# Kernel tuning notes

Hardware: AMD Instinct MI355X
Metric: run time of the kernel (lower is better)

The kernel has to match this reference:

```python
import jax, jax.numpy as jnp
import numpy as np

SEQ, B, XD = 2048, 4, 16
D, NH, DFF, L, M = 256, 8, 512, 2, 1024
DH = D // NH
NEG_INF = -1e9  # finite stand-in for -inf (same softmax result, grad-safe)


def setup_inputs() -> dict:
    key = jax.random.key(0)
    ks = iter(jax.random.split(key, 40))

    def w(shape, s=0.02):
        return jax.random.normal(next(ks), shape, dtype=jnp.float32) * s

    return {
        "x": jax.random.normal(next(ks), (SEQ, B, XD), dtype=jnp.float32),
        "y": jax.random.normal(next(ks), (SEQ, B), dtype=jnp.float32),
        "single_eval_pos": M,
        "xenc_w": w((D, XD)), "xenc_b": w((D,)),
        "yenc_w": w((D, 1)), "yenc_b": w((D,)),
        "in_proj_w": w((L, 3 * D, D)), "in_proj_b": w((L, 3 * D)),
        "out_proj_w": w((L, D, D)), "out_proj_b": w((L, D)),
        "ln1_g": jnp.ones((L, D), jnp.float32), "ln1_b": jnp.zeros((L, D), jnp.float32),
        "lin1_w": w((L, DFF, D)), "lin1_b": w((L, DFF)),
        "lin2_w": w((L, D, DFF)), "lin2_b": w((L, D)),
        "ln2_g": jnp.ones((L, D), jnp.float32), "ln2_b": jnp.zeros((L, D), jnp.float32),
        "head_w1": w((DFF, D)), "head_b1": w((DFF,)),
        "head_w2": w((1, DFF)), "head_b2": w((1,)),
    }


def _layer_norm(x, g, b, eps=1e-5):
    mu = jnp.mean(x, axis=-1, keepdims=True)
    var = jnp.var(x, axis=-1, keepdims=True)
    return (x - mu) * jax.lax.rsqrt(var + eps) * g + b


def _forward(x, y, M_, p):
    seq, batch = y.shape
    x_src = x @ p["xenc_w"].T + p["xenc_b"]                     # [seq, b, D]
    y_src = y[..., None] @ p["yenc_w"].T + p["yenc_b"]           # [seq, b, D]
    tokens = jnp.concatenate([x_src[:M_] + y_src[:M_], x_src[M_:]], axis=0)

    # prefix-block + diagonal mask: keep (j < M) or (i == j)
    i = jnp.arange(seq)
    keep = (i[None, :] < M_) | (i[:, None] == i[None, :])
    mask = jnp.where(keep, 0.0, NEG_INF).astype(tokens.dtype)    # [seq, seq]

    h = tokens
    for l in range(p["in_proj_w"].shape[0]):
        qkv = h @ p["in_proj_w"][l].T + p["in_proj_b"][l]        # [seq, b, 3D]
        q, k, v = jnp.split(qkv, 3, axis=-1)
        to_heads = lambda t: t.reshape(seq, batch, NH, DH).transpose(1, 2, 0, 3)
        q, k, v = to_heads(q), to_heads(k), to_heads(v)          # [b, h, s, dh]
        scores = jnp.einsum("bhqd,bhkd->bhqk", q, k) / np.float32(np.sqrt(DH)) + mask
        attn = jax.nn.softmax(scores, axis=-1)
        o = jnp.einsum("bhqk,bhkd->bhqd", attn, v)
        o = o.transpose(2, 0, 1, 3).reshape(seq, batch, D)
        o = o @ p["out_proj_w"][l].T + p["out_proj_b"][l]
        h = _layer_norm(h + o, p["ln1_g"][l], p["ln1_b"][l])      # post-norm
        ff = jax.nn.gelu(h @ p["lin1_w"][l].T + p["lin1_b"][l], approximate=False)
        ff = ff @ p["lin2_w"][l].T + p["lin2_b"][l]
        h = _layer_norm(h + ff, p["ln2_g"][l], p["ln2_b"][l])

    q_out = h[M_:]                                               # [seq-M, b, D]
    hid = jax.nn.gelu(q_out @ p["head_w1"].T + p["head_b1"], approximate=False)
    return hid @ p["head_w2"].T + p["head_b2"]                   # [seq-M, b, 1]


def reference(x, y, single_eval_pos, xenc_w, xenc_b, yenc_w, yenc_b,
              in_proj_w, in_proj_b, out_proj_w, out_proj_b,
              ln1_g, ln1_b, lin1_w, lin1_b, lin2_w, lin2_b, ln2_g, ln2_b,
              head_w1, head_b1, head_w2, head_b2):
    p = dict(xenc_w=xenc_w, xenc_b=xenc_b, yenc_w=yenc_w, yenc_b=yenc_b,
             in_proj_w=in_proj_w, in_proj_b=in_proj_b,
             out_proj_w=out_proj_w, out_proj_b=out_proj_b,
             ln1_g=ln1_g, ln1_b=ln1_b, lin1_w=lin1_w, lin1_b=lin1_b,
             lin2_w=lin2_w, lin2_b=lin2_b, ln2_g=ln2_g, ln2_b=ln2_b,
             head_w1=head_w1, head_b1=head_b1, head_w2=head_w2, head_b2=head_b2)
    return _forward(x, y, int(single_eval_pos), p)
```

## Files before the change

kernel.cpp:

```cpp
#include <hip/hip_runtime.h>
#include <hip/hip_bf16.h>
#include <math.h>

#define SEQ    2048
#define BATCH  4
#define XDIM   16
#define DMODEL 256
#define NHEAD  8
#define DH     32
#define DFF    512
#define NLAYER 2
#define MPOS   1024
#define ROWS   (SEQ*BATCH)

#define ATT_SCALE 0.17677669529663687f

typedef __attribute__((ext_vector_type(8))) short bf16x8;
typedef __attribute__((ext_vector_type(4))) float f32x4;

__device__ __forceinline__ float gelu_exact(float x) {
    return 0.5f * x * (1.0f + erff(x * 0.70710678118654752f));
}
__device__ __forceinline__ short f2bf(float f) {
    unsigned int u = __float_as_uint(f);
    u += 0x7FFFu + ((u >> 16) & 1u);
    return (short)(u >> 16);
}
__device__ __forceinline__ float bf2f(unsigned short u) {
    return __uint_as_float(((unsigned int)u) << 16);
}
__device__ __forceinline__ void gload16(const unsigned short* g, unsigned short* l) {
    __builtin_amdgcn_global_load_lds(
        (const __attribute__((address_space(1))) unsigned int*)g,
        (__attribute__((address_space(3))) unsigned int*)l, 16, 0, 0);
}
#define VMWAIT(N) asm volatile("s_waitcnt vmcnt(" #N ")" ::: "memory")
__device__ __forceinline__ void pipe_barrier() {
    __builtin_amdgcn_sched_barrier(0);
    __builtin_amdgcn_s_barrier();
    __builtin_amdgcn_sched_barrier(0);
}

__global__ __launch_bounds__(256) void encode_cast(
    const float* __restrict__ x, const float* __restrict__ y,
    const float* __restrict__ xw, const float* __restrict__ xb,
    const float* __restrict__ yw, const float* __restrict__ yb,
    float* __restrict__ h, unsigned short* __restrict__ hb,
    const float* __restrict__ s0, const float* __restrict__ s1,
    const float* __restrict__ s2, const float* __restrict__ s3,
    const float* __restrict__ s4,
    unsigned short* __restrict__ d0, unsigned short* __restrict__ d1,
    unsigned short* __restrict__ d2, unsigned short* __restrict__ d3,
    unsigned short* __restrict__ d4)
{
    if (blockIdx.x < ROWS/4) {
        int g = blockIdx.x;
        int d = threadIdx.x;
        __shared__ float xs[4][XDIM];
        __shared__ float ys[4];
        if (d < 64) xs[d>>4][d&15] = x[(size_t)(g*4 + (d>>4))*XDIM + (d&15)];
        if (d < 4)  ys[d] = y[g*4 + d];
        __syncthreads();
        float wreg[XDIM];
        #pragma unroll
        for (int k = 0; k < XDIM; ++k) wreg[k] = xw[d*XDIM + k];
        const float xbv = xb[d], ywv = yw[d], ybv = yb[d];
        const bool train = (g < MPOS);
        #pragma unroll
        for (int r = 0; r < 4; ++r) {
            int row = g*4 + r;
            float acc = xbv;
            #pragma unroll
            for (int k = 0; k < XDIM; ++k) acc = fmaf(xs[r][k], wreg[k], acc);
            if (train) acc += ys[r]*ywv + ybv;
            h[(size_t)row*DMODEL + d]  = acc;
            hb[(size_t)row*DMODEL + d] = (unsigned short)f2bf(acc);
        }
        return;
    }
    int i = (blockIdx.x - ROWS/4)*256 + threadIdx.x;
    if (i >= 147456) return;
    const float* s; unsigned short* d; int off;
    if      (i <  49152) { s = s0; d = d0; off = i; }
    else if (i <  65536) { s = s1; d = d1; off = i - 49152; }
    else if (i <  98304) { s = s2; d = d2; off = i - 65536; }
    else if (i < 131072) { s = s3; d = d3; off = i - 98304; }
    else                 { s = s4; d = d4; off = i - 131072; }
    float4 a = *(const float4*)(s + (size_t)off*8);
    float4 c = *(const float4*)(s + (size_t)off*8 + 4);
    ushort4 u0, u1;
    u0.x=(unsigned short)f2bf(a.x); u0.y=(unsigned short)f2bf(a.y);
    u0.z=(unsigned short)f2bf(a.z); u0.w=(unsigned short)f2bf(a.w);
    u1.x=(unsigned short)f2bf(c.x); u1.y=(unsigned short)f2bf(c.y);
    u1.z=(unsigned short)f2bf(c.z); u1.w=(unsigned short)f2bf(c.w);
    *(ushort4*)(d + (size_t)off*8)     = u0;
    *(ushort4*)(d + (size_t)off*8 + 4) = u1;
}

__global__ __launch_bounds__(512) void gemm_qkv(
    const unsigned short* __restrict__ A, const unsigned short* __restrict__ B,
    const float* __restrict__ bias,
    unsigned short* __restrict__ Qg, unsigned short* __restrict__ Kg,
    unsigned short* __restrict__ Vg, int K)
{
    __shared__ unsigned short As[2][128][64];
    __shared__ unsigned short Bs[2][64][64];
    int tid  = threadIdx.x;
    int w    = tid >> 6, lane = tid & 63;
    int col  = lane & 15, quad = lane >> 4;
    int wr   = w >> 1, wc = w & 1;
    int u    = blockIdx.x >> 3, xcd = blockIdx.x & 7;
    int by   = xcd*8 + u/12, bx = u%12;
    int m0   = by * 128, n0 = bx * 64;
    int l8   = lane >> 3;
    int c8s  = (((lane & 7) ^ l8) * 8);

    f32x4 acc[2][2];
    #pragma unroll
    for (int i = 0; i < 2; ++i)
        #pragma unroll
        for (int j = 0; j < 2; ++j) acc[i][j] = (f32x4){0.f,0.f,0.f,0.f};

    const unsigned short* ga = A + (size_t)(m0 + w*16 + l8)*K + c8s;
    const unsigned short* gb = B + (size_t)(n0 + w*8  + l8)*K + c8s;
    const int NS = K / 64;

    gload16(ga,                 &As[0][w*16    ][0]);
    gload16(ga + (size_t)8*K,   &As[0][w*16 + 8][0]);
    gload16(gb,                 &Bs[0][w*8     ][0]);

    for (int s = 0; s < NS; ++s) {
        VMWAIT(0);
        pipe_barrier();
        if (s + 1 < NS) {
            int k2 = (s + 1) * 64;
            int nb = (s + 1) & 1;
            gload16(ga + k2,               &As[nb][w*16    ][0]);
            gload16(ga + k2 + (size_t)8*K, &As[nb][w*16 + 8][0]);
            gload16(gb + k2,               &Bs[nb][w*8     ][0]);
        }
        int cur = s & 1;
        #pragma unroll
        for (int kk = 0; kk < 2; ++kk) {
            const int so = (((kk*4 + quad) ^ (col & 7)) * 8);
            bf16x8 af[2], bfr[2];
            #pragma unroll
            for (int i = 0; i < 2; ++i) af[i]  = *(const bf16x8*)&As[cur][wr*32 + i*16 + col][so];
            #pragma unroll
            for (int j = 0; j < 2; ++j) bfr[j] = *(const bf16x8*)&Bs[cur][wc*32 + j*16 + col][so];
            #pragma unroll
            for (int i = 0; i < 2; ++i)
                #pragma unroll
                for (int j = 0; j < 2; ++j)
                    acc[i][j] = __builtin_amdgcn_mfma_f32_16x16x32_bf16(bfr[j], af[i], acc[i][j], 0, 0, 0);
        }
    }

    int region = n0 >> 8;
    if (region < 2) {
        #pragma unroll
        for (int i = 0; i < 2; ++i) {
            int m = m0 + wr*32 + i*16 + col;
            int s = m >> 2, bidx = m & 3;
            #pragma unroll
            for (int j = 0; j < 2; ++j) {
                int ng = n0 + wc*32 + j*16 + quad*4;
                float4 bi = *(const float4*)&bias[ng];
                ushort4 uu;
                uu.x=(unsigned short)f2bf(acc[i][j][0] + bi.x);
                uu.y=(unsigned short)f2bf(acc[i][j][1] + bi.y);
                uu.z=(unsigned short)f2bf(acc[i][j][2] + bi.z);
                uu.w=(unsigned short)f2bf(acc[i][j][3] + bi.w);
                int np = ng - (region << 8);
                int hh = np >> 5, d = np & 31;
                int bh = bidx*NHEAD + hh;
                if (region == 0)
                    *(ushort4*)(Qg + ((size_t)(bh*SEQ + s))*DH + d) = uu;
                else
                    *(ushort4*)(Kg + ((size_t)(bh*SEQ + s))*DH + d) = uu;
            }
        }
    } else {
        __syncthreads();
        unsigned short* T3 = (unsigned short*)As;
        #pragma unroll
        for (int i = 0; i < 2; ++i) {
            int mi = wr*32 + i*16 + col;
            int ss = mi >> 2, bidx = mi & 3;
            #pragma unroll
            for (int j = 0; j < 2; ++j) {
                int ni = wc*32 + j*16 + quad*4;
                float4 bi = *(const float4*)&bias[n0 + ni];
                T3[((ni    )*4 + bidx)*32 + ss] = (unsigned short)f2bf(acc[i][j][0] + bi.x);
                T3[((ni + 1)*4 + bidx)*32 + ss] = (unsigned short)f2bf(acc[i][j][1] + bi.y);
                T3[((ni + 2)*4 + bidx)*32 + ss] = (unsigned short)f2bf(acc[i][j][2] + bi.z);
                T3[((ni + 3)*4 + bidx)*32 + ss] = (unsigned short)f2bf(acc[i][j][3] + bi.w);
            }
        }
        __syncthreads();
        int sBase = m0 >> 2;
        #pragma unroll
        for (int r = 0; r < 2; ++r) {
            int chunk = tid + 512*r;
            int l = chunk >> 2, p = chunk & 3;
            int d = l & 31, hh_l = (l >> 5) & 1, bidx = l >> 6;
            int ni = hh_l*32 + d;
            int hh = ((n0 & 255) + ni) >> 5;
            int bh = bidx*NHEAD + hh;
            uint4 val = *(const uint4*)&T3[(ni*4 + bidx)*32 + p*8];
            *(uint4*)(Vg + ((size_t)(bh*DH + d))*SEQ + sBase + p*8) = val;
        }
    }
}

__global__ __launch_bounds__(512) void attn_mfma(
    const unsigned short* __restrict__ Qg,
    const unsigned short* __restrict__ Kg,
    const unsigned short* __restrict__ Vg,
    unsigned short* __restrict__ o)
{
    const int id  = blockIdx.x;
    const int sl  = id >> 3;
    const int bh  = (id & 7) * 4 + (sl >> 4);
    const int qt2 = sl & 15;
    const int h   = bh & 7;
    const int b   = bh >> 3;
    const int q0A = qt2 * 64;
    const int q0B = MPOS + qt2 * 64;
    const int tid  = threadIdx.x;
    const int w    = tid >> 6;
    const int ws   = w & 3;
    const int grp  = w >> 2;
    const int lane = tid & 63;
    const int col  = lane & 15;
    const int quad = lane >> 4;

    __shared__ unsigned short Kt[2][128][40];
    __shared__ unsigned short Vt[2][32][136];
    __shared__ unsigned short Pt[8][16][136];

    const int q0 = grp ? q0B : q0A;
    const int q  = q0 + 16*ws + col;
    bf16x8 qf = *(const bf16x8*)(Qg + ((size_t)(bh*SEQ + q))*DH + quad*8);

    f32x4 O0 = {0.f,0.f,0.f,0.f};
    f32x4 O1 = {0.f,0.f,0.f,0.f};
    float lsum = 0.f;

    const int kRow = tid >> 2,  kCh = (tid & 3) * 8;
    const int vD   = tid >> 4,  vCh = (tid & 15) * 8;

    uint4 kreg = *(const uint4*)(Kg + ((size_t)(bh*SEQ + kRow))*DH + kCh);
    uint4 vreg = *(const uint4*)(Vg + ((size_t)(bh*DH + vD))*SEQ + vCh);

    for (int kt = 0; kt < 8; ++kt) {
        const int p = kt & 1;
        *(uint4*)&Kt[p][kRow][kCh] = kreg;
        *(uint4*)&Vt[p][vD][vCh]   = vreg;
        __syncthreads();
        if (kt < 7) {
            int kn = (kt + 1) * 128;
            kreg = *(const uint4*)(Kg + ((size_t)(bh*SEQ + kn + kRow))*DH + kCh);
            vreg = *(const uint4*)(Vg + ((size_t)(bh*DH + vD))*SEQ + kn + vCh);
        } else {
            if (kRow < 64)
                kreg = *(const uint4*)(Kg + ((size_t)(bh*SEQ + q0B + kRow))*DH + kCh);
            if (vCh < 64)
                vreg = *(const uint4*)(Vg + ((size_t)(bh*DH + vD))*SEQ + q0B + vCh);
        }

        #pragma unroll
        for (int mt = 0; mt < 8; ++mt) {
            bf16x8 kf = *(const bf16x8*)&Kt[p][mt*16 + col][quad*8];
            f32x4 st = {0.f,0.f,0.f,0.f};
            st = __builtin_amdgcn_mfma_f32_16x16x32_bf16(kf, qf, st, 0, 0, 0);
            ushort4 pw;
            #pragma unroll
            for (int i = 0; i < 4; ++i) {
                float pv = __expf(st[i]*ATT_SCALE);
                unsigned short us = (unsigned short)f2bf(pv);
                ((unsigned short*)&pw)[i] = us;
                lsum += bf2f(us);
            }
            *(ushort4*)&Pt[w][col][mt*16 + quad*4] = pw;
        }
        #pragma unroll
        for (int c = 0; c < 4; ++c) {
            bf16x8 v0 = *(const bf16x8*)&Vt[p][col     ][c*32 + quad*8];
            bf16x8 v1 = *(const bf16x8*)&Vt[p][col + 16][c*32 + quad*8];
            bf16x8 pf = *(const bf16x8*)&Pt[w][col][c*32 + quad*8];
            O0 = __builtin_amdgcn_mfma_f32_16x16x32_bf16(v0, pf, O0, 0, 0, 0);
            O1 = __builtin_amdgcn_mfma_f32_16x16x32_bf16(v1, pf, O1, 0, 0, 0);
        }
    }

    if (kRow < 64) *(uint4*)&Kt[0][kRow][kCh] = kreg;
    if (vCh < 64)  *(uint4*)&Vt[0][vD][vCh]   = vreg;
    __syncthreads();
    if (grp == 1) {
        #pragma unroll
        for (int mt = 0; mt < 4; ++mt) {
            bf16x8 kf = *(const bf16x8*)&Kt[0][mt*16 + col][quad*8];
            f32x4 st = {0.f,0.f,0.f,0.f};
            st = __builtin_amdgcn_mfma_f32_16x16x32_bf16(kf, qf, st, 0, 0, 0);
            ushort4 pw;
            #pragma unroll
            for (int i = 0; i < 4; ++i) {
                float pv = __expf(st[i]*ATT_SCALE);
                if (mt*16 + quad*4 + i != 16*ws + col) pv = 0.f;
                unsigned short us = (unsigned short)f2bf(pv);
                ((unsigned short*)&pw)[i] = us;
                lsum += bf2f(us);
            }
            *(ushort4*)&Pt[w][col][mt*16 + quad*4] = pw;
        }
        #pragma unroll
        for (int c = 0; c < 2; ++c) {
            bf16x8 v0 = *(const bf16x8*)&Vt[0][col     ][c*32 + quad*8];
            bf16x8 v1 = *(const bf16x8*)&Vt[0][col + 16][c*32 + quad*8];
            bf16x8 pf = *(const bf16x8*)&Pt[w][col][c*32 + quad*8];
            O0 = __builtin_amdgcn_mfma_f32_16x16x32_bf16(v0, pf, O0, 0, 0, 0);
            O1 = __builtin_amdgcn_mfma_f32_16x16x32_bf16(v1, pf, O1, 0, 0, 0);
        }
    }

    lsum += __shfl_xor(lsum, 16, 64);
    lsum += __shfl_xor(lsum, 32, 64);
    float inv = 1.0f / lsum;
    ushort4 u0, u1;
    #pragma unroll
    for (int i = 0; i < 4; ++i) {
        ((unsigned short*)&u0)[i] = (unsigned short)f2bf(O0[i]*inv);
        ((unsigned short*)&u1)[i] = (unsigned short)f2bf(O1[i]*inv);
    }
    unsigned short* op = o + ((size_t)(q*BATCH + b))*DMODEL + h*DH;
    *(ushort4*)(op + quad*4)      = u0;
    *(ushort4*)(op + 16 + quad*4) = u1;
}

__global__ __launch_bounds__(512) void mlp_fused(
    const unsigned short* __restrict__ attb,
    const unsigned short* __restrict__ Wout, const float* __restrict__ ob,
    const float* __restrict__ g1, const float* __restrict__ be1,
    const unsigned short* __restrict__ W1, const float* __restrict__ fb1,
    const unsigned short* __restrict__ W2, const float* __restrict__ fb2,
    const float* __restrict__ g2, const float* __restrict__ be2,
    float* __restrict__ h, unsigned short* __restrict__ hb,
    const unsigned short* __restrict__ Wh1, const float* __restrict__ hb1,
    const float* __restrict__ hw2, const float* __restrict__ hb2,
    float* __restrict__ out, int doHead)
{
    __shared__ unsigned short Bs[3][256][64];
    __shared__ __align__(16) unsigned char smem_u[33280];
    __shared__ unsigned short Ht[2][16][264];
    __shared__ float sP[2][8][16], qP[2][8][16];

    typedef unsigned short AsT[2][16][64];
    AsT* As = reinterpret_cast<AsT*>(smem_u);
    typedef unsigned short PtT[16][520];
    PtT* Pt = reinterpret_cast<PtT*>(smem_u);

    const int tid  = threadIdx.x;
    const int w    = tid >> 6;
    const int lane = tid & 63;
    const int col  = lane & 15;
    const int quad = lane >> 4;
    const int l8   = lane >> 3;
    const int c8s  = (((lane & 7) ^ l8) * 8);
    const int bid  = blockIdx.x;
    const int m0a  = bid * 16;
    const int m0b  = 4096 + bid * 16;
    const int ma   = m0a + col;
    const int mb   = m0b + col;

    float resid[2][2][4];

    {
        f32x4 acc[2][2];
        #pragma unroll
        for (int g = 0; g < 2; ++g)
            #pragma unroll
            for (int j = 0; j < 2; ++j) acc[g][j] = (f32x4){0.f,0.f,0.f,0.f};

        const int gr = w >> 1;
        const unsigned short* gaw = attb + (size_t)((gr ? m0b : m0a) + (w&1)*8 + l8)*DMODEL + c8s;
        const unsigned short* gb  = Wout + (size_t)(w*32 + l8)*DMODEL + c8s;
        const int NS = DMODEL / 64;

        #pragma unroll
        for (int pb = 0; pb < 2; ++pb) {
            int k = pb * 64;
            if (w < 4) gload16(gaw + k, &As[pb][gr][(w&1)*8][0]);
            #pragma unroll
            for (int t = 0; t < 4; ++t)
                gload16(gb + k + (size_t)(t*8)*DMODEL, &Bs[pb][w*32 + t*8][0]);
        }
        int bcur = 0;
        for (int s = 0; s < NS; ++s) {
            if (s == NS - 1)      { VMWAIT(0); }
            else if (w < 4)       { VMWAIT(5); }
            else                  { VMWAIT(4); }
            pipe_barrier();
            if (s + 2 < NS) {
                int bpre = bcur + 2; if (bpre >= 3) bpre -= 3;
                int k2 = (s + 2) * 64;
                if (w < 4) gload16(gaw + k2, &As[bpre][gr][(w&1)*8][0]);
                #pragma unroll
                for (int t = 0; t < 4; ++t)
                    gload16(gb + k2 + (size_t)(t*8)*DMODEL, &Bs[bpre][w*32 + t*8][0]);
            }
            #pragma unroll
            for (int kk = 0; kk < 2; ++kk) {
                const int so = (((kk*4 + quad) ^ (col & 7)) * 8);
                bf16x8 af0 = *(const bf16x8*)&As[bcur][0][col][so];
                bf16x8 af1 = *(const bf16x8*)&As[bcur][1][col][so];
                #pragma unroll
                for (int j = 0; j < 2; ++j) {
                    bf16x8 bfr = *(const bf16x8*)&Bs[bcur][w*32 + j*16 + col][so];
                    acc[0][j] = __builtin_amdgcn_mfma_f32_16x16x32_bf16(bfr, af0, acc[0][j], 0, 0, 0);
                    acc[1][j] = __builtin_amdgcn_mfma_f32_16x16x32_bf16(bfr, af1, acc[1][j], 0, 0, 0);
                }
            }
            bcur = (bcur == 2) ? 0 : bcur + 1;
        }

        float ssum[2] = {0.f, 0.f}, qsum[2] = {0.f, 0.f};
        #pragma unroll
        for (int g = 0; g < 2; ++g) {
            int m = g ? mb : ma;
            #pragma unroll
            for (int j = 0; j < 2; ++j) {
                int n = w*32 + j*16 + quad*4;
                float4 bi = *(const float4*)&ob[n];
                float4 hv = *(const float4*)&h[(size_t)m*DMODEL + n];
                #pragma unroll
                for (int i = 0; i < 4; ++i) {
                    float val = acc[g][j][i] + ((const float*)&bi)[i] + ((const float*)&hv)[i];
                    resid[g][j][i] = val;
                    ssum[g] += val; qsum[g] += val*val;
                }
            }
        }
        #pragma unroll
        for (int g = 0; g < 2; ++g) {
            ssum[g] += __shfl_xor(ssum[g], 16, 64); ssum[g] += __shfl_xor(ssum[g], 32, 64);
            qsum[g] += __shfl_xor(qsum[g], 16, 64); qsum[g] += __shfl_xor(qsum[g], 32, 64);
        }
        if (quad == 0) {
            sP[0][w][col] = ssum[0]; qP[0][w][col] = qsum[0];
            sP[1][w][col] = ssum[1]; qP[1][w][col] = qsum[1];
        }
        __syncthreads();
        #pragma unroll
        for (int g = 0; g < 2; ++g) {
            float st = 0.f, qt = 0.f;
            #pragma unroll
            for (int ww = 0; ww < 8; ++ww) { st += sP[g][ww][col]; qt += qP[g][ww][col]; }
            float mu   = st * (1.0f/DMODEL);
            float var  = qt * (1.0f/DMODEL) - mu*mu;
            float rstd = rsqrtf(var + 1e-5f);
            #pragma unroll
            for (int j = 0; j < 2; ++j) {
                int n = w*32 + j*16 + quad*4;
                float4 gv = *(const float4*)&g1[n];
                float4 bv = *(const float4*)&be1[n];
                ushort4 u;
                #pragma unroll
                for (int i = 0; i < 4; ++i) {
                    float o = (resid[g][j][i]-mu)*rstd*((const float*)&gv)[i] + ((const float*)&bv)[i];
                    resid[g][j][i] = o;
                    ((unsigned short*)&u)[i] = (unsigned short)f2bf(o);
                }
                *(ushort4*)&Ht[g][col][n] = u;
            }
        }
        __syncthreads();
    }

    #pragma unroll 1
    for (int nh = 0; nh < 2; ++nh) {
        f32x4 acc[2][2];
        #pragma unroll
        for (int g = 0; g < 2; ++g)
            #pragma unroll
            for (int j = 0; j < 2; ++j) acc[g][j] = (f32x4){0.f,0.f,0.f,0.f};
        const unsigned short* gb = W1 + (size_t)(nh*256 + w*32 + l8)*DMODEL + c8s;
        const int NS = DMODEL / 64;

        #pragma unroll
        for (int pb = 0; pb < 2; ++pb)
            #pragma unroll
            for (int t = 0; t < 4; ++t)
                gload16(gb + pb*64 + (size_t)(t*8)*DMODEL, &Bs[pb][w*32 + t*8][0]);

        int bcur = 0;
        for (int s = 0; s < NS; ++s) {
            if (s == NS - 1) { VMWAIT(0); } else { VMWAIT(4); }
            if (s + 2 < NS) {
                int bpre = bcur + 2; if (bpre >= 3) bpre -= 3;
                int k2 = (s + 2) * 64;
                #pragma unroll
                for (int t = 0; t < 4; ++t)
                    gload16(gb + k2 + (size_t)(t*8)*DMODEL, &Bs[bpre][w*32 + t*8][0]);
            }
            #pragma unroll
            for (int kk = 0; kk < 2; ++kk) {
                const int so = (((kk*4 + quad) ^ (col & 7)) * 8);
                bf16x8 af0 = *(const bf16x8*)&Ht[0][col][s*64 + kk*32 + quad*8];
                bf16x8 af1 = *(const bf16x8*)&Ht[1][col][s*64 + kk*32 + quad*8];
                #pragma unroll
                for (int j = 0; j < 2; ++j) {
                    bf16x8 bfr = *(const bf16x8*)&Bs[bcur][w*32 + j*16 + col][so];
                    acc[0][j] = __builtin_amdgcn_mfma_f32_16x16x32_bf16(bfr, af0, acc[0][j], 0, 0, 0);
                    acc[1][j] = __builtin_amdgcn_mfma_f32_16x16x32_bf16(bfr, af1, acc[1][j], 0, 0, 0);
                }
            }
            bcur = (bcur == 2) ? 0 : bcur + 1;
        }
        #pragma unroll
        for (int g = 0; g < 2; ++g)
            #pragma unroll
            for (int j = 0; j < 2; ++j) {
                int n2 = nh*256 + w*32 + j*16 + quad*4;
                float4 bi = *(const float4*)&fb1[n2];
                ushort4 u;
                #pragma unroll
                for (int i = 0; i < 4; ++i)
                    ((unsigned short*)&u)[i] = (unsigned short)f2bf(gelu_exact(acc[g][j][i] + ((const float*)&bi)[i]));
                *(ushort4*)&Pt[g][col][n2] = u;
            }
    }

    {
        __syncthreads();
        f32x4 acc[2][2];
        #pragma unroll
        for (int g = 0; g < 2; ++g)
            #pragma unroll
            for (int j = 0; j < 2; ++j) acc[g][j] = (f32x4){0.f,0.f,0.f,0.f};
        const unsigned short* gb = W2 + (size_t)(w*32 + l8)*DFF + c8s;
        const int NS = DFF / 64;

        #pragma unroll
        for (int pb = 0; pb < 2; ++pb)
            #pragma unroll
            for (int t = 0; t < 4; ++t)
                gload16(gb + pb*64 + (size_t)(t*8)*DFF, &Bs[pb][w*32 + t*8][0]);

        int bcur = 0;
        for (int s = 0; s < NS; ++s) {
            if (s == NS - 1) { VMWAIT(0); } else { VMWAIT(4); }
            if (s + 2 < NS) {
                int bpre = bcur + 2; if (bpre >= 3) bpre -= 3;
                int k2 = (s + 2) * 64;
                #pragma unroll
                for (int t = 0; t < 4; ++t)
                    gload16(gb + k2 + (size_t)(t*8)*DFF, &Bs[bpre][w*32 + t*8][0]);
            }
            #pragma unroll
            for (int kk = 0; kk < 2; ++kk) {
                const int so = (((kk*4 + quad) ^ (col & 7)) * 8);
                bf16x8 af0 = *(const bf16x8*)&Pt[0][col][s*64 + kk*32 + quad*8];
                bf16x8 af1 = *(const bf16x8*)&Pt[1][col][s*64 + kk*32 + quad*8];
                #pragma unroll
                for (int j = 0; j < 2; ++j) {
                    bf16x8 bfr = *(const bf16x8*)&Bs[bcur][w*32 + j*16 + col][so];
                    acc[0][j] = __builtin_amdgcn_mfma_f32_16x16x32_bf16(bfr, af0, acc[0][j], 0, 0, 0);
                    acc[1][j] = __builtin_amdgcn_mfma_f32_16x16x32_bf16(bfr, af1, acc[1][j], 0, 0, 0);
                }
            }
            bcur = (bcur == 2) ? 0 : bcur + 1;
        }

        float ssum[2] = {0.f, 0.f}, qsum[2] = {0.f, 0.f};
        #pragma unroll
        for (int g = 0; g < 2; ++g)
            #pragma unroll
            for (int j = 0; j < 2; ++j) {
                int n = w*32 + j*16 + quad*4;
                float4 bi = *(const float4*)&fb2[n];
                #pragma unroll
                for (int i = 0; i < 4; ++i) {
                    float val = acc[g][j][i] + ((const float*)&bi)[i] + resid[g][j][i];
                    resid[g][j][i] = val;
                    ssum[g] += val; qsum[g] += val*val;
                }
            }
        #pragma unroll
        for (int g = 0; g < 2; ++g) {
            ssum[g] += __shfl_xor(ssum[g], 16, 64); ssum[g] += __shfl_xor(ssum[g], 32, 64);
            qsum[g] += __shfl_xor(qsum[g], 16, 64); qsum[g] += __shfl_xor(qsum[g], 32, 64);
        }
        if (quad == 0) {
            sP[0][w][col] = ssum[0]; qP[0][w][col] = qsum[0];
            sP[1][w][col] = ssum[1]; qP[1][w][col] = qsum[1];
        }
        __syncthreads();
        #pragma unroll
        for (int g = 0; g < 2; ++g) {
            int m = g ? mb : ma;
            float st = 0.f, qt = 0.f;
            #pragma unroll
            for (int ww = 0; ww < 8; ++ww) { st += sP[g][ww][col]; qt += qP[g][ww][col]; }
            float mu   = st * (1.0f/DMODEL);
            float var  = qt * (1.0f/DMODEL) - mu*mu;
            float rstd = rsqrtf(var + 1e-5f);
            #pragma unroll
            for (int j = 0; j < 2; ++j) {
                int n = w*32 + j*16 + quad*4;
                float4 gv = *(const float4*)&g2[n];
                float4 bv = *(const float4*)&be2[n];
                float4 o;
                ushort4 u;
                #pragma unroll
                for (int i = 0; i < 4; ++i) {
                    float ov = (resid[g][j][i]-mu)*rstd*((const float*)&gv)[i] + ((const float*)&bv)[i];
                    ((float*)&o)[i] = ov;
                    ((unsigned short*)&u)[i] = (unsigned short)f2bf(ov);
                }
                *(float4*)&h[(size_t)m*DMODEL + n] = o;
                *(ushort4*)(hb + (size_t)m*DMODEL + n) = u;
                *(ushort4*)&Ht[g][col][n] = u;
            }
        }
        __syncthreads();
    }

    if (doHead) {
        float sdot = 0.f;
        #pragma unroll 1
        for (int nh = 0; nh < 2; ++nh) {
            f32x4 acc[2];
            #pragma unroll
            for (int j = 0; j < 2; ++j) acc[j] = (f32x4){0.f,0.f,0.f,0.f};
            const unsigned short* gb = Wh1 + (size_t)(nh*256 + w*32 + l8)*DMODEL + c8s;
            const int NS = DMODEL / 64;

            #pragma unroll
            for (int pb = 0; pb < 2; ++pb)
                #pragma unroll
                for (int t = 0; t < 4; ++t)
                    gload16(gb + pb*64 + (size_t)(t*8)*DMODEL, &Bs[pb][w*32 + t*8][0]);

            int bcur = 0;
            for (int s = 0; s < NS; ++s) {
                if (s == NS - 1) { VMWAIT(0); } else { VMWAIT(4); }
                if (s + 2 < NS) {
                    int bpre = bcur + 2; if (bpre >= 3) bpre -= 3;
                    int k2 = (s + 2) * 64;
                    #pragma unroll
                    for (int t = 0; t < 4; ++t)
                        gload16(gb + k2 + (size_t)(t*8)*DMODEL, &Bs[bpre][w*32 + t*8][0]);
                }
                #pragma unroll
                for (int kk = 0; kk < 2; ++kk) {
                    const int so = (((kk*4 + quad) ^ (col & 7)) * 8);
                    bf16x8 af = *(const bf16x8*)&Ht[1][col][s*64 + kk*32 + quad*8];
                    #pragma unroll
                    for (int j = 0; j < 2; ++j) {
                        bf16x8 bfr = *(const bf16x8*)&Bs[bcur][w*32 + j*16 + col][so];
                        acc[j] = __builtin_amdgcn_mfma_f32_16x16x32_bf16(bfr, af, acc[j], 0, 0, 0);
                    }
                }
                bcur = (bcur == 2) ? 0 : bcur + 1;
            }
            #pragma unroll
            for (int j = 0; j < 2; ++j) {
                int n2 = nh*256 + w*32 + j*16 + quad*4;
                float4 b1v = *(const float4*)&hb1[n2];
                float4 w2v = *(const float4*)&hw2[n2];
                #pragma unroll
                for (int i = 0; i < 4; ++i)
                    sdot += gelu_exact(acc[j][i] + ((const float*)&b1v)[i]) * ((const float*)&w2v)[i];
            }
        }
        sdot += __shfl_xor(sdot, 16, 64); sdot += __shfl_xor(sdot, 32, 64);
        if (quad == 0) sP[0][w][col] = sdot;
        __syncthreads();
        if (tid < 16) {
            float r = hb2[0];
            #pragma unroll
            for (int ww = 0; ww < 8; ++ww) r += sP[0][ww][tid];
            out[bid*16 + tid] = r;
        }
    }
}

extern "C" void kernel_launch(void* const* d_in, const int* in_sizes, int n_in,
                              void* d_out, int out_size, void* d_ws, size_t ws_size,
                              hipStream_t stream)
{
    const float* x        = (const float*)d_in[0];
    const float* y        = (const float*)d_in[1];
    const float* xenc_w   = (const float*)d_in[3];
    const float* xenc_b   = (const float*)d_in[4];
    const float* yenc_w   = (const float*)d_in[5];
    const float* yenc_b   = (const float*)d_in[6];
    const float* in_proj_w  = (const float*)d_in[7];
    const float* in_proj_b  = (const float*)d_in[8];
    const float* out_proj_w = (const float*)d_in[9];
    const float* out_proj_b = (const float*)d_in[10];
    const float* ln1_g    = (const float*)d_in[11];
    const float* ln1_b    = (const float*)d_in[12];
    const float* lin1_w   = (const float*)d_in[13];
    const float* lin1_b   = (const float*)d_in[14];
    const float* lin2_w   = (const float*)d_in[15];
    const float* lin2_b   = (const float*)d_in[16];
    const float* ln2_g    = (const float*)d_in[17];
    const float* ln2_b    = (const float*)d_in[18];
    const float* head_w1  = (const float*)d_in[19];
    const float* head_b1  = (const float*)d_in[20];
    const float* head_w2  = (const float*)d_in[21];
    const float* head_b2  = (const float*)d_in[22];
    float* out = (float*)d_out;

    float* ws  = (float*)d_ws;
    float* h    = ws;
    unsigned short* hb    = (unsigned short*)(h + (size_t)ROWS*DMODEL);
    unsigned short* attb  = hb    + (size_t)ROWS*DMODEL;
    unsigned short* Qg    = attb  + (size_t)ROWS*DMODEL;
    unsigned short* Kg    = Qg    + (size_t)BATCH*NHEAD*SEQ*DH;
    unsigned short* Vg    = Kg    + (size_t)BATCH*NHEAD*SEQ*DH;
    unsigned short* Wqkv  = Vg    + (size_t)BATCH*NHEAD*SEQ*DH;
    unsigned short* Wout  = Wqkv  + (size_t)NLAYER*3*DMODEL*DMODEL;
    unsigned short* Wl1   = Wout  + (size_t)NLAYER*DMODEL*DMODEL;
    unsigned short* Wl2   = Wl1   + (size_t)NLAYER*DFF*DMODEL;
    unsigned short* Wh1   = Wl2   + (size_t)NLAYER*DMODEL*DFF;

    encode_cast<<<ROWS/4 + 576, 256, 0, stream>>>(
        x, y, xenc_w, xenc_b, yenc_w, yenc_b, h, hb,
        in_proj_w, out_proj_w, lin1_w, lin2_w, head_w1,
        Wqkv, Wout, Wl1, Wl2, Wh1);

    for (int l = 0; l < NLAYER; ++l) {
        gemm_qkv<<<768, 512, 0, stream>>>(
            hb, Wqkv + (size_t)l*3*DMODEL*DMODEL, in_proj_b + l*3*DMODEL,
            Qg, Kg, Vg, DMODEL);
        attn_mfma<<<512, 512, 0, stream>>>(Qg, Kg, Vg, attb);
        mlp_fused<<<256, 512, 0, stream>>>(
            attb,
            Wout + (size_t)l*DMODEL*DMODEL, out_proj_b + l*DMODEL,
            ln1_g + l*DMODEL, ln1_b + l*DMODEL,
            Wl1 + (size_t)l*DFF*DMODEL, lin1_b + l*DFF,
            Wl2 + (size_t)l*DMODEL*DFF, lin2_b + l*DMODEL,
            ln2_g + l*DMODEL, ln2_b + l*DMODEL,
            h, hb,
            Wh1, head_b1, head_w2, head_b2,
            out, (l == NLAYER-1) ? 1 : 0);
    }
}
```

Baseline: 222.9 us.

## Preload full B tile in QKV GEMM and give each wave private A rows

The QKV projection GEMM now loads the whole 64x256 B (weight) slice into shared memory once up front. Each wave then streams its own 16 rows of A into a private shared buffer, which removes the per-iteration block-wide barrier and the B double-buffering. Each wave computes a 16x64 output strip with four MFMAs per k-chunk instead of a 2x2 layout. The cost is larger shared-memory use per block and waves that no longer share A fragments, and the V-transpose epilogue now relies on T3 aliasing the resized As buffer.

```diff
diff --git a/kernel.cpp b/kernel.cpp
--- a/kernel.cpp
+++ b/kernel.cpp
@@ -103,99 +103,94 @@
     unsigned short* __restrict__ Qg, unsigned short* __restrict__ Kg,
     unsigned short* __restrict__ Vg, int K)
 {
-    __shared__ unsigned short As[2][128][64];
-    __shared__ unsigned short Bs[2][64][64];
+    __shared__ unsigned short Bsf[4][64][64];
+    __shared__ unsigned short As[8][16][64];
     int tid  = threadIdx.x;
     int w    = tid >> 6, lane = tid & 63;
     int col  = lane & 15, quad = lane >> 4;
-    int wr   = w >> 1, wc = w & 1;
     int u    = blockIdx.x >> 3, xcd = blockIdx.x & 7;
     int by   = xcd*8 + u/12, bx = u%12;
     int m0   = by * 128, n0 = bx * 64;
     int l8   = lane >> 3;
     int c8s  = (((lane & 7) ^ l8) * 8);
 
-    f32x4 acc[2][2];
+    f32x4 acc[4];
     #pragma unroll
-    for (int i = 0; i < 2; ++i)
-        #pragma unroll
-        for (int j = 0; j < 2; ++j) acc[i][j] = (f32x4){0.f,0.f,0.f,0.f};
+    for (int j = 0; j < 4; ++j) acc[j] = (f32x4){0.f,0.f,0.f,0.f};
 
     const unsigned short* ga = A + (size_t)(m0 + w*16 + l8)*K + c8s;
-    const unsigned short* gb = B + (size_t)(n0 + w*8  + l8)*K + c8s;
     const int NS = K / 64;
 
-    gload16(ga,                 &As[0][w*16    ][0]);
-    gload16(ga + (size_t)8*K,   &As[0][w*16 + 8][0]);
-    gload16(gb,                 &Bs[0][w*8     ][0]);
+    {
+        int seg = w >> 1;
+        int r0  = (w & 1) * 32;
+        const unsigned short* gbw = B + (size_t)(n0 + r0 + l8)*K + seg*64 + c8s;
+        #pragma unroll
+        for (int t = 0; t < 4; ++t)
+            gload16(gbw + (size_t)(t*8)*K, &Bsf[seg][r0 + t*8][0]);
+    }
+    gload16(ga,               &As[w][0][0]);
+    gload16(ga + (size_t)8*K, &As[w][8][0]);
+    VMWAIT(0);
+    pipe_barrier();
 
     for (int s = 0; s < NS; ++s) {
-        VMWAIT(0);
-        pipe_barrier();
+        if (s > 0) VMWAIT(0);
+        bf16x8 af0 = *(const bf16x8*)&As[w][col][(((0*4 + quad) ^ (col & 7)) * 8)];
+        bf16x8 af1 = *(const bf16x8*)&As[w][col][(((1*4 + quad) ^ (col & 7)) * 8)];
+        asm volatile("s_waitcnt lgkmcnt(0)" ::: "memory");
+        __builtin_amdgcn_sched_barrier(0);
         if (s + 1 < NS) {
             int k2 = (s + 1) * 64;
-            int nb = (s + 1) & 1;
-            gload16(ga + k2,               &As[nb][w*16    ][0]);
-            gload16(ga + k2 + (size_t)8*K, &As[nb][w*16 + 8][0]);
-            gload16(gb + k2,               &Bs[nb][w*8     ][0]);
-        }
-        int cur = s & 1;
+            gload16(ga + k2,               &As[w][0][0]);
+            gload16(ga + k2 + (size_t)8*K, &As[w][8][0]);
+        }
         #pragma unroll
         for (int kk = 0; kk < 2; ++kk) {
             const int so = (((kk*4 + quad) ^ (col & 7)) * 8);
-            bf16x8 af[2], bfr[2];
-            #pragma unroll
-            for (int i = 0; i < 2; ++i) af[i]  = *(const bf16x8*)&As[cur][wr*32 + i*16 + col][so];
-            #pragma unroll
-            for (int j = 0; j < 2; ++j) bfr[j] = *(const bf16x8*)&Bs[cur][wc*32 + j*16 + col][so];
-            #pragma unroll
-            for (int i = 0; i < 2; ++i)
-                #pragma unroll
-                for (int j = 0; j < 2; ++j)
-                    acc[i][j] = __builtin_amdgcn_mfma_f32_16x16x32_bf16(bfr[j], af[i], acc[i][j], 0, 0, 0);
+            bf16x8 af = kk ? af1 : af0;
+            #pragma unroll
+            for (int j = 0; j < 4; ++j) {
+                bf16x8 bfr = *(const bf16x8*)&Bsf[s][j*16 + col][so];
+                acc[j] = __builtin_amdgcn_mfma_f32_16x16x32_bf16(bfr, af, acc[j], 0, 0, 0);
+            }
         }
     }
 
     int region = n0 >> 8;
     if (region < 2) {
-        #pragma unroll
-        for (int i = 0; i < 2; ++i) {
-            int m = m0 + wr*32 + i*16 + col;
-            int s = m >> 2, bidx = m & 3;
-            #pragma unroll
-            for (int j = 0; j < 2; ++j) {
-                int ng = n0 + wc*32 + j*16 + quad*4;
-                float4 bi = *(const float4*)&bias[ng];
-                ushort4 uu;
-                uu.x=(unsigned short)f2bf(acc[i][j][0] + bi.x);
-                uu.y=(unsigned short)f2bf(acc[i][j][1] + bi.y);
-                uu.z=(unsigned short)f2bf(acc[i][j][2] + bi.z);
-                uu.w=(unsigned short)f2bf(acc[i][j][3] + bi.w);
-                int np = ng - (region << 8);
-                int hh = np >> 5, d = np & 31;
-                int bh = bidx*NHEAD + hh;
-                if (region == 0)
-                    *(ushort4*)(Qg + ((size_t)(bh*SEQ + s))*DH + d) = uu;
-                else
-                    *(ushort4*)(Kg + ((size_t)(bh*SEQ + s))*DH + d) = uu;
-            }
+        int m = m0 + w*16 + col;
+        int s = m >> 2, bidx = m & 3;
+        #pragma unroll
+        for (int j = 0; j < 4; ++j) {
+            int ng = n0 + j*16 + quad*4;
+            float4 bi = *(const float4*)&bias[ng];
+            ushort4 uu;
+            uu.x=(unsigned short)f2bf(acc[j][0] + bi.x);
+            uu.y=(unsigned short)f2bf(acc[j][1] + bi.y);
+            uu.z=(unsigned short)f2bf(acc[j][2] + bi.z);
+            uu.w=(unsigned short)f2bf(acc[j][3] + bi.w);
+            int np = ng - (region << 8);
+            int hh = np >> 5, d = np & 31;
+            int bh = bidx*NHEAD + hh;
+            if (region == 0)
+                *(ushort4*)(Qg + ((size_t)(bh*SEQ + s))*DH + d) = uu;
+            else
+                *(ushort4*)(Kg + ((size_t)(bh*SEQ + s))*DH + d) = uu;
         }
     } else {
         __syncthreads();
         unsigned short* T3 = (unsigned short*)As;
-        #pragma unroll
-        for (int i = 0; i < 2; ++i) {
-            int mi = wr*32 + i*16 + col;
-            int ss = mi >> 2, bidx = mi & 3;
-            #pragma unroll
-            for (int j = 0; j < 2; ++j) {
-                int ni = wc*32 + j*16 + quad*4;
-                float4 bi = *(const float4*)&bias[n0 + ni];
-                T3[((ni    )*4 + bidx)*32 + ss] = (unsigned short)f2bf(acc[i][j][0] + bi.x);
-                T3[((ni + 1)*4 + bidx)*32 + ss] = (unsigned short)f2bf(acc[i][j][1] + bi.y);
-                T3[((ni + 2)*4 + bidx)*32 + ss] = (unsigned short)f2bf(acc[i][j][2] + bi.z);
-                T3[((ni + 3)*4 + bidx)*32 + ss] = (unsigned short)f2bf(acc[i][j][3] + bi.w);
-            }
+        int mi = w*16 + col;
+        int ss = mi >> 2, bidx = mi & 3;
+        #pragma unroll
+        for (int j = 0; j < 4; ++j) {
+            int ni = j*16 + quad*4;
+            float4 bi = *(const float4*)&bias[n0 + ni];
+            T3[((ni    )*4 + bidx)*32 + ss] = (unsigned short)f2bf(acc[j][0] + bi.x);
+            T3[((ni + 1)*4 + bidx)*32 + ss] = (unsigned short)f2bf(acc[j][1] + bi.y);
+            T3[((ni + 2)*4 + bidx)*32 + ss] = (unsigned short)f2bf(acc[j][2] + bi.z);
+            T3[((ni + 3)*4 + bidx)*32 + ss] = (unsigned short)f2bf(acc[j][3] + bi.w);
         }
         __syncthreads();
         int sBase = m0 >> 2;
@@ -203,11 +198,11 @@
         for (int r = 0; r < 2; ++r) {
             int chunk = tid + 512*r;
             int l = chunk >> 2, p = chunk & 3;
-            int d = l & 31, hh_l = (l >> 5) & 1, bidx = l >> 6;
+            int d = l & 31, hh_l = (l >> 5) & 1, bidx2 = l >> 6;
             int ni = hh_l*32 + d;
             int hh = ((n0 & 255) + ni) >> 5;
-            int bh = bidx*NHEAD + hh;
-            uint4 val = *(const uint4*)&T3[(ni*4 + bidx)*32 + p*8];
+            int bh = bidx2*NHEAD + hh;
+            uint4 val = *(const uint4*)&T3[(ni*4 + bidx2)*32 + p*8];
             *(uint4*)(Vg + ((size_t)(bh*DH + d))*SEQ + sBase + p*8) = val;
         }
     }
```

New measurement: 225.6 us, median of 2. About the same (+1.2%).
